# Kernel optimization log

Hardware: AMD Instinct MI355X
Metric: run time of the kernel (lower is better)

Reference implementation:

```python
import jax, jax.numpy as jnp
import numpy as np

GAMMA = 0.96875
SCALE_BASE = 512.0


def _fixed_pos_embedding(scale):
    # scale: (L, d) where d = head_dim // 2
    L, d = scale.shape
    inv_freq = 1.0 / (10000.0 ** (jnp.arange(d, dtype=jnp.float32) / d))
    sinusoid = jnp.arange(L, dtype=jnp.float32)[:, None] * inv_freq  # (L, d)
    return jnp.sin(sinusoid), jnp.cos(sinusoid)


def _rotate_every_two(x):
    # (..., D) -> (..., D) with pairs (x0, x1) -> (-x1, x0)
    x1 = x[..., ::2]
    x2 = x[..., 1::2]
    return jnp.stack((-x2, x1), axis=-1).reshape(x.shape)


def _dup_interleave(m):
    # (L, d) -> (L, 2d), each column duplicated (matches rotary pairing)
    return jnp.repeat(m, 2, axis=-1)


def xpos(x, offset=0, downscale=False):
    # x: (B, S, D). Standard torchscale-style XPos rotary embedding.
    S, D = x.shape[-2], x.shape[-1]
    scale_vec = (jnp.arange(0, D, 2, dtype=jnp.float32) + 0.4 * D) / (1.4 * D)  # (D/2,)
    min_pos = -(S + offset) // 2
    max_pos = S + offset + min_pos
    power = jnp.arange(min_pos, max_pos, dtype=jnp.float32) / SCALE_BASE  # (S+offset,)
    scale = scale_vec ** power[:, None]  # (S+offset, D/2)
    sin, cos = _fixed_pos_embedding(scale)
    if scale.shape[0] > S:  # keep the last S positions
        scale, sin, cos = scale[-S:], sin[-S:], cos[-S:]
    if downscale:
        scale = 1.0 / scale
    sin = _dup_interleave(sin * scale)  # (S, D)
    cos = _dup_interleave(cos * scale)  # (S, D)
    return x * cos + _rotate_every_two(x) * sin


def _decay_mask(S, dtype):
    # D[n, m] = gamma^(n-m) if n >= m else 0  (lower triangular)
    m = jnp.arange(S)
    diff = m[:, None] - m  # (S, S)
    causal = diff >= 0
    exp = jnp.where(causal, diff, 0).astype(dtype)
    return jnp.where(causal, jnp.asarray(GAMMA, dtype) ** exp, jnp.zeros((), dtype))


def setup_inputs() -> dict:
    key = jax.random.key(0)
    kx, kq, kk, kv = jax.random.split(key, 4)
    B, S, H, Dh = 4, 4096, 2048, 256
    return {
        "x": jax.random.normal(kx, (B, S, H), dtype=jnp.float32),
        "w_q": jax.random.normal(kq, (H, Dh), dtype=jnp.float32),
        "w_k": jax.random.normal(kk, (H, Dh), dtype=jnp.float32),
        "w_v": jax.random.normal(kv, (H, Dh), dtype=jnp.float32),
    }


def reference(x, w_q, w_k, w_v):
    # x: (B, S, H) -> out: (B, S, Dh)
    B, S, _ = x.shape
    decay = _decay_mask(S, x.dtype)[None]  # (1, S, S)
    q = xpos(x @ w_q)                       # (B, S, Dh)
    k = xpos(x @ w_k, downscale=True)       # (B, S, Dh)
    v = x @ w_v                             # (B, S, Dh)
    ret = jnp.einsum("bsd,btd->bst", q, k) * decay  # (B, S, S)
    return jnp.einsum("bst,btd->bsd", ret, v)       # (B, S, Dh)
```

## Files before the change

### kernel.cpp

```cpp
#include <hip/hip_runtime.h>
#include <cstddef>
#include <cstdint>

#define Bn 4
#define Sn 4096
#define Hn 2048
#define Dn 256

typedef float f32x16 __attribute__((ext_vector_type(16)));
typedef short bf16x8 __attribute__((ext_vector_type(8)));

#define AS3 __attribute__((address_space(3)))
#define AS1 __attribute__((address_space(1)))

#define L2G -0.045803689613125f
#define GC 2.9526131e-4f

__device__ __forceinline__ unsigned short f2bf(float f) {
  union { float f; unsigned int u; } a; a.f = f;
  unsigned int r = a.u + 0x7fffu + ((a.u >> 16) & 1u);
  return (unsigned short)(r >> 16);
}
__device__ __forceinline__ float bf2f(unsigned int b) {
  union { unsigned int u; float f; } a; a.u = b << 16;
  return a.f;
}

__global__ __launch_bounds__(256) void prep_kernel(const float* __restrict__ x,
                                                   const float* __restrict__ wq,
                                                   const float* __restrict__ wk,
                                                   const float* __restrict__ wv,
                                                   unsigned short* __restrict__ xb,
                                                   unsigned short* __restrict__ wt,
                                                   float* __restrict__ rt) {
  __shared__ __align__(16) unsigned short T[64][72];
  const int bx = blockIdx.x;
  const int tid = threadIdx.x;
  if (bx < 2048) {
    const int g = bx * 256 + tid;
    const int s = g >> 7;
    const int jp = g & 127;
    const float invf = exp2f((float)jp * (-13.287712379549449f / 128.0f));
    float sn, cs;
    sincosf((float)s * invf, &sn, &cs);
    const float l2sv = log2f((2.0f * jp + 102.4f) * (1.0f / 358.4f));
    const float pw = ((float)s - 2048.0f) * (1.0f / 512.0f);
    const float tl = (float)(s & 255) * L2G;
    const float ex = pw * l2sv + tl;
    const float eq = exp2f(ex), ek = exp2f(-ex);
    float2* q = (float2*)rt;
    float2* k = (float2*)(rt + 4096 * 256);
    q[(size_t)s * 128 + jp] = make_float2(cs * eq, sn * eq);
    k[(size_t)s * 128 + jp] = make_float2(cs * ek, sn * ek);
  } else if (bx < 10240) {
    const size_t g = (size_t)(bx - 2048) * 256 + tid;
    const float* src = x + g * 16;
    unsigned short* dst = xb + g * 16;
    uint4 o0, o1;
    float4 v0 = ((const float4*)src)[0];
    float4 v1 = ((const float4*)src)[1];
    float4 v2 = ((const float4*)src)[2];
    float4 v3 = ((const float4*)src)[3];
    o0.x = f2bf(v0.x) | ((unsigned int)f2bf(v0.y) << 16);
    o0.y = f2bf(v0.z) | ((unsigned int)f2bf(v0.w) << 16);
    o0.z = f2bf(v1.x) | ((unsigned int)f2bf(v1.y) << 16);
    o0.w = f2bf(v1.z) | ((unsigned int)f2bf(v1.w) << 16);
    o1.x = f2bf(v2.x) | ((unsigned int)f2bf(v2.y) << 16);
    o1.y = f2bf(v2.z) | ((unsigned int)f2bf(v2.w) << 16);
    o1.z = f2bf(v3.x) | ((unsigned int)f2bf(v3.y) << 16);
    o1.w = f2bf(v3.z) | ((unsigned int)f2bf(v3.w) << 16);
    ((uint4*)dst)[0] = o0;
    ((uint4*)dst)[1] = o1;
  } else {
    const int bw = bx - 10240;
    const int k0 = (bw & 31) * 64;
    const int n0 = (bw >> 5) * 64;
    const float* w = (n0 < 256) ? wq : (n0 < 512 ? wk : wv);
    const int nc0 = n0 & 255;
#pragma unroll
    for (int it = 0; it < 2; ++it) {
      int flat = it * 256 + tid;
      int r = flat >> 3, c8 = flat & 7;
      const float* src = w + (size_t)(k0 + r) * 256 + nc0 + c8 * 8;
      float4 v0 = *(const float4*)src;
      float4 v1 = *(const float4*)(src + 4);
      T[c8 * 8 + 0][r] = f2bf(v0.x); T[c8 * 8 + 1][r] = f2bf(v0.y);
      T[c8 * 8 + 2][r] = f2bf(v0.z); T[c8 * 8 + 3][r] = f2bf(v0.w);
      T[c8 * 8 + 4][r] = f2bf(v1.x); T[c8 * 8 + 5][r] = f2bf(v1.y);
      T[c8 * 8 + 6][r] = f2bf(v1.z); T[c8 * 8 + 7][r] = f2bf(v1.w);
    }
    __syncthreads();
#pragma unroll
    for (int it = 0; it < 2; ++it) {
      int flat = it * 256 + tid;
      int nr = flat >> 3, kc8 = flat & 7;
      int n = n0 + nr;
      int kc_sw = kc8 ^ (n & 7);
      uint4 val = *(const uint4*)&T[nr][kc8 * 8];
      *(uint4*)((char*)wt + (size_t)n * 4096 + (size_t)k0 * 2 + kc_sw * 16) = val;
    }
  }
}

__global__ __launch_bounds__(512, 2) void proj4_kernel(const unsigned short* __restrict__ xb,
                                                       const unsigned short* __restrict__ wt,
                                                       const float* __restrict__ rt,
                                                       unsigned short* __restrict__ qkv,
                                                       unsigned short* __restrict__ kt,
                                                       unsigned short* __restrict__ vt) {
  __shared__ __align__(16) char smem[49152];
  unsigned short* As = (unsigned short*)smem;
  unsigned short* Bs = (unsigned short*)(smem + 16384);
  const int tid = threadIdx.x;
  const int lane = tid & 63;
  const int wid = tid >> 6;
  const int wr = wid >> 2, wc = wid & 3;
  const int m0 = blockIdx.x * 128;
  const int kind = blockIdx.y;
  const int l31 = lane & 31, lh = lane >> 5;

  f32x16 acc[2][2];
#pragma unroll
  for (int i = 0; i < 2; ++i)
#pragma unroll
    for (int j = 0; j < 2; ++j) acc[i][j] = 0.0f;

  for (int k0 = 0; k0 < Hn; k0 += 64) {
    AS3 char* ldsa = (AS3 char*)As;
    AS3 char* ldsb = (AS3 char*)Bs;
#pragma unroll
    for (int i = 0; i < 2; ++i) {
      int ou = i * 8192 + wid * 1024;
      int o = ou + lane * 16;
      int row = o >> 7, colB = o & 127;
      const char* srcA = (const char*)xb + (size_t)(m0 + row) * 4096 + k0 * 2 + (colB ^ ((row & 7) << 4));
      __builtin_amdgcn_global_load_lds((const AS1 unsigned int*)srcA,
                                       (AS3 unsigned int*)(ldsa + ou), 16, 0, 0);
    }
#pragma unroll
    for (int i = 0; i < 4; ++i) {
      int ou = i * 8192 + wid * 1024;
      int o = ou + lane * 16;
      int row = o >> 7, colB = o & 127;
      const char* srcB = (const char*)wt + (size_t)(kind * 256 + row) * 4096 + k0 * 2 + colB;
      __builtin_amdgcn_global_load_lds((const AS1 unsigned int*)srcB,
                                       (AS3 unsigned int*)(ldsb + ou), 16, 0, 0);
    }
    __syncthreads();
#pragma unroll
    for (int kc = 0; kc < 4; ++kc) {
      const int kb = kc * 32 + lh * 16;
      bf16x8 a[2], b[2];
#pragma unroll
      for (int i = 0; i < 2; ++i) {
        int mr = wr * 64 + i * 32 + l31;
        a[i] = *(const bf16x8*)((const char*)As + mr * 128 + (kb ^ ((mr & 7) << 4)));
        int nr = wc * 64 + i * 32 + l31;
        b[i] = *(const bf16x8*)((const char*)Bs + nr * 128 + (kb ^ ((nr & 7) << 4)));
      }
#pragma unroll
      for (int i = 0; i < 2; ++i)
#pragma unroll
        for (int j = 0; j < 2; ++j)
          acc[i][j] = __builtin_amdgcn_mfma_f32_32x32x16_bf16(a[i], b[j], acc[i][j], 0, 0, 0);
    }
    __syncthreads();
  }

  const int bidx = m0 >> 12;
  const int t0b = m0 & 4095;

  if (kind < 2) {
    const float* rtb = rt + (size_t)kind * (4096 * 256);
    int jp[2];
#pragma unroll
    for (int j = 0; j < 2; ++j) jp[j] = (wc * 64 + j * 32 + l31) >> 1;
    const int odd = l31 & 1;
#pragma unroll
    for (int i = 0; i < 2; ++i)
#pragma unroll
      for (int reg = 0; reg < 16; ++reg) {
        const int mm = m0 + wr * 64 + i * 32 + (reg & 3) + 8 * (reg >> 2) + 4 * lh;
        const int s = mm & (Sn - 1);
#pragma unroll
        for (int j = 0; j < 2; ++j) {
          const float2 cf = *(const float2*)(rtb + (size_t)s * 256 + jp[j] * 2);
          float v = acc[i][j][reg];
          float p = __shfl_xor(v, 1, 64);
          acc[i][j][reg] = odd ? (v * cf.x + p * cf.y) : (v * cf.x - p * cf.y);
        }
      }
  }

  if (kind == 0) {
#pragma unroll
    for (int i = 0; i < 2; ++i)
#pragma unroll
      for (int j = 0; j < 2; ++j)
#pragma unroll
        for (int reg = 0; reg < 16; ++reg) {
          int m = m0 + wr * 64 + i * 32 + (reg & 3) + 8 * (reg >> 2) + 4 * lh;
          int n = wc * 64 + j * 32 + l31;
          qkv[(size_t)m * 768 + n] = f2bf(acc[i][j][reg]);
        }
  } else {
    if (kind == 1) {
#pragma unroll
      for (int i = 0; i < 2; ++i)
#pragma unroll
        for (int j = 0; j < 2; ++j)
#pragma unroll
          for (int reg = 0; reg < 16; ++reg) {
            int m = m0 + wr * 64 + i * 32 + (reg & 3) + 8 * (reg >> 2) + 4 * lh;
            int d = wc * 64 + j * 32 + l31;
            qkv[(size_t)m * 768 + 256 + (d ^ ((m & 7) << 3))] = f2bf(acc[i][j][reg]);
          }
    }
    unsigned short* dst = (kind == 1) ? kt : vt;
#pragma unroll
    for (int h = 0; h < 2; ++h) {
      __syncthreads();
      if ((wc >> 1) == h) {
#pragma unroll
        for (int i = 0; i < 2; ++i)
#pragma unroll
          for (int j = 0; j < 2; ++j) {
            const int dl = (wc & 1) * 64 + j * 32 + l31;
#pragma unroll
            for (int k8 = 0; k8 < 8; ++k8) {
              const int r0 = 2 * k8;
              const int t = wr * 64 + i * 32 + (r0 & 3) + 8 * (r0 >> 2) + 4 * lh;
              unsigned int pk;
              asm("v_cvt_pk_bf16_f32 %0, %1, %2" : "=v"(pk)
                  : "v"(acc[i][j][r0]), "v"(acc[i][j][r0 + 1]));
              *(unsigned int*)(smem + dl * 256 + ((2 * t) ^ ((dl & 7) << 4))) = pk;
            }
          }
      }
      __syncthreads();
#pragma unroll
      for (int p = 0; p < 4; ++p) {
        const int fl = p * 512 + tid;
        const int dl = fl >> 4, t8 = fl & 15;
        uint4 val = *(const uint4*)(smem + dl * 256 + ((t8 * 16) ^ ((dl & 7) << 4)));
        *(uint4*)(dst + (size_t)(bidx * 256 + h * 128 + dl) * 4096 + t0b + t8 * 8) = val;
      }
    }
  }
}

__global__ __launch_bounds__(256) void wt_build(const float* __restrict__ wq,
                                                const float* __restrict__ wk,
                                                const float* __restrict__ wv,
                                                unsigned short* __restrict__ wt) {
  __shared__ __align__(16) unsigned short T[64][72];
  const int tid = threadIdx.x;
  const int k0 = blockIdx.x * 64;
  const int n0 = blockIdx.y * 64;
  const float* w = (n0 < 256) ? wq : (n0 < 512 ? wk : wv);
  const int nc0 = n0 & 255;
#pragma unroll
  for (int it = 0; it < 2; ++it) {
    int flat = it * 256 + tid;
    int r = flat >> 3, c8 = flat & 7;
    const float* src = w + (size_t)(k0 + r) * 256 + nc0 + c8 * 8;
    float4 v0 = *(const float4*)src;
    float4 v1 = *(const float4*)(src + 4);
    T[c8 * 8 + 0][r] = f2bf(v0.x); T[c8 * 8 + 1][r] = f2bf(v0.y);
    T[c8 * 8 + 2][r] = f2bf(v0.z); T[c8 * 8 + 3][r] = f2bf(v0.w);
    T[c8 * 8 + 4][r] = f2bf(v1.x); T[c8 * 8 + 5][r] = f2bf(v1.y);
    T[c8 * 8 + 6][r] = f2bf(v1.z); T[c8 * 8 + 7][r] = f2bf(v1.w);
  }
  __syncthreads();
#pragma unroll
  for (int it = 0; it < 2; ++it) {
    int flat = it * 256 + tid;
    int nr = flat >> 3, kc8 = flat & 7;
    int n = n0 + nr;
    int kc_sw = kc8 ^ (n & 7);
    uint4 val = *(const uint4*)&T[nr][kc8 * 8];
    *(uint4*)((char*)wt + (size_t)n * 4096 + (size_t)k0 * 2 + kc_sw * 16) = val;
  }
}

__global__ __launch_bounds__(256, 2) void proj_kernel(const float* __restrict__ x,
                                                      const unsigned short* __restrict__ wt,
                                                      unsigned short* __restrict__ qkv) {
  __shared__ __align__(16) unsigned short As[128 * 64];
  __shared__ __align__(16) unsigned short Bs[128 * 64];
  const int tid = threadIdx.x;
  const int lane = tid & 63;
  const int wid = tid >> 6;
  const int wr = wid >> 1, wc = wid & 1;
  const int m0 = blockIdx.x * 128;
  const int n0 = blockIdx.y * 128;
  const int l31 = lane & 31, lh = lane >> 5;

  f32x16 acc[2][2];
#pragma unroll
  for (int i = 0; i < 2; ++i)
#pragma unroll
    for (int j = 0; j < 2; ++j) acc[i][j] = 0.0f;

  for (int k0 = 0; k0 < Hn; k0 += 64) {
    {
      AS3 char* ldsb = (AS3 char*)Bs;
#pragma unroll
      for (int i = 0; i < 4; ++i) {
        int ou = i * 4096 + wid * 1024;
        int o = ou + lane * 16;
        int row = o >> 7, col = o & 127;
        const char* src = (const char*)wt + (size_t)(n0 + row) * 4096 + k0 * 2 + col;
        __builtin_amdgcn_global_load_lds((const AS1 unsigned int*)src,
                                         (AS3 unsigned int*)(ldsb + ou), 16, 0, 0);
      }
    }
#pragma unroll
    for (int i = 0; i < 4; ++i) {
      int o = i * 256 + tid;
      int row = o >> 3, c8 = o & 7;
      const float* src = x + (size_t)(m0 + row) * 2048 + k0 + c8 * 8;
      float4 v0 = *(const float4*)src;
      float4 v1 = *(const float4*)(src + 4);
      uint4 val;
      val.x = f2bf(v0.x) | ((unsigned int)f2bf(v0.y) << 16);
      val.y = f2bf(v0.z) | ((unsigned int)f2bf(v0.w) << 16);
      val.z = f2bf(v1.x) | ((unsigned int)f2bf(v1.y) << 16);
      val.w = f2bf(v1.z) | ((unsigned int)f2bf(v1.w) << 16);
      *(uint4*)((char*)As + row * 128 + ((c8 * 16) ^ ((row & 7) << 4))) = val;
    }
    __syncthreads();
#pragma unroll
    for (int kc = 0; kc < 4; ++kc) {
      const int kb = kc * 32 + lh * 16;
      bf16x8 a[2], b[2];
#pragma unroll
      for (int i = 0; i < 2; ++i) {
        int mr = wr * 64 + i * 32 + l31;
        a[i] = *(const bf16x8*)((const char*)As + mr * 128 + (kb ^ ((mr & 7) << 4)));
        int nr = wc * 64 + i * 32 + l31;
        b[i] = *(const bf16x8*)((const char*)Bs + nr * 128 + (kb ^ ((nr & 7) << 4)));
      }
#pragma unroll
      for (int i = 0; i < 2; ++i)
#pragma unroll
        for (int j = 0; j < 2; ++j)
          acc[i][j] = __builtin_amdgcn_mfma_f32_32x32x16_bf16(a[i], b[j], acc[i][j], 0, 0, 0);
    }
    __syncthreads();
  }
  const bool khalf = (n0 >= 256 && n0 < 512);
#pragma unroll
  for (int i = 0; i < 2; ++i)
#pragma unroll
    for (int j = 0; j < 2; ++j)
#pragma unroll
      for (int reg = 0; reg < 16; ++reg) {
        int m = m0 + wr * 64 + i * 32 + (reg & 3) + 8 * (reg >> 2) + 4 * lh;
        int n = n0 + wc * 64 + j * 32 + l31;
        if (khalf) n = 256 + ((n - 256) ^ ((m & 7) << 3));
        qkv[(size_t)m * 768 + n] = f2bf(acc[i][j][reg]);
      }
}

__global__ __launch_bounds__(256) void xpos_kernel(unsigned short* __restrict__ qkv) {
  const int g = blockIdx.x * 256 + threadIdx.x;
  const int m = g >> 5;
  const int c = g & 31;
  const float s = (float)(m & (Sn - 1));
  unsigned short* qrow = qkv + (size_t)m * 768;
  const int csw = c ^ (m & 7);
  uint4 qv = *(uint4*)(qrow + c * 8);
  uint4 kv = *(uint4*)(qrow + 256 + csw * 8);
  unsigned int* qu = (unsigned int*)&qv;
  unsigned int* ku = (unsigned int*)&kv;
  const float pw = (s - 2048.0f) * (1.0f / 512.0f);
  const float gp = exp2f((float)(m & 255) * L2G);
#pragma unroll
  for (int p = 0; p < 4; ++p) {
    const int jp = c * 4 + p;
    const float invf = exp2f((float)jp * (-13.287712379549449f / 128.0f));
    float sn, cs;
    sincosf(s * invf, &sn, &cs);
    const float sv = (2.0f * jp + 102.4f) * (1.0f / 358.4f);
    const float scq = exp2f(pw * log2f(sv)) * gp;
    const float sci = 1.0f / scq;
    float q0 = bf2f(qu[p] & 0xffffu), q1 = bf2f(qu[p] >> 16);
    float k0 = bf2f(ku[p] & 0xffffu), k1 = bf2f(ku[p] >> 16);
    float q0r = (q0 * cs - q1 * sn) * scq;
    float q1r = (q1 * cs + q0 * sn) * scq;
    float k0r = (k0 * cs - k1 * sn) * sci;
    float k1r = (k1 * cs + k0 * sn) * sci;
    qu[p] = f2bf(q0r) | ((unsigned int)f2bf(q1r) << 16);
    ku[p] = f2bf(k0r) | ((unsigned int)f2bf(k1r) << 16);
  }
  *(uint4*)(qrow + c * 8) = qv;
  *(uint4*)(qrow + 256 + csw * 8) = kv;
}

__global__ __launch_bounds__(256) void kvt_build(const unsigned short* __restrict__ qkv,
                                                 unsigned short* __restrict__ kt,
                                                 unsigned short* __restrict__ vt) {
  __shared__ __align__(16) unsigned short Tk[64][72];
  __shared__ __align__(16) unsigned short Tv[64][72];
  const int tid = threadIdx.x;
  const int t0 = blockIdx.x * 64;
  const int d0 = blockIdx.y * 64;
  const int b = blockIdx.z;
  const size_t rowb = ((size_t)b * Sn + t0) * 1536;
#pragma unroll
  for (int it = 0; it < 2; ++it) {
    int flat = it * 256 + tid;
    int r = flat >> 3, c8 = flat & 7;
    int kc = (d0 >> 3) + c8;
    int kcs = kc ^ (r & 7);
    uint4 kvv = *(const uint4*)((const char*)qkv + rowb + (size_t)r * 1536 + 512 + kcs * 16);
    uint4 vvv = *(const uint4*)((const char*)qkv + rowb + (size_t)r * 1536 + 1024 + (size_t)(d0 + c8 * 8) * 2);
    const unsigned short* ke = (const unsigned short*)&kvv;
    const unsigned short* ve = (const unsigned short*)&vvv;
#pragma unroll
    for (int e = 0; e < 8; ++e) { Tk[c8 * 8 + e][r] = ke[e]; Tv[c8 * 8 + e][r] = ve[e]; }
  }
  __syncthreads();
#pragma unroll
  for (int it = 0; it < 2; ++it) {
    int flat = it * 256 + tid;
    int dr = flat >> 3, tc8 = flat & 7;
    *(uint4*)(kt + (size_t)(b * 256 + d0 + dr) * 4096 + t0 + tc8 * 8) = *(const uint4*)&Tk[dr][tc8 * 8];
    *(uint4*)(vt + (size_t)(b * 256 + d0 + dr) * 4096 + t0 + tc8 * 8) = *(const uint4*)&Tv[dr][tc8 * 8];
  }
}

__global__ __launch_bounds__(256) void mbuild_kernel(const unsigned short* __restrict__ kt,
                                                     const unsigned short* __restrict__ vt,
                                                     unsigned short* __restrict__ mt) {
  const int tid = threadIdx.x;
  const int lane = tid & 63;
  const int wid = tid >> 6;
  const int l31 = lane & 31, lh = lane >> 5;
  const int jc = blockIdx.x;
  const int quad = blockIdx.y;
  const int b = blockIdx.z;
  const int d2w = ((quad >> 1) * 2 + (wid >> 1)) * 64;
  const int d1w = ((quad & 1) * 2 + (wid & 1)) * 64;
  const size_t tb = (size_t)jc * 256;

  f32x16 acc[2][2];
#pragma unroll
  for (int i = 0; i < 2; ++i)
#pragma unroll
    for (int j = 0; j < 2; ++j) acc[i][j] = 0.0f;

#pragma unroll 2
  for (int dc = 0; dc < 16; ++dc) {
    const int ko = dc * 32 + lh * 16;
    bf16x8 a[2], bb[2];
#pragma unroll
    for (int i = 0; i < 2; ++i) {
      a[i]  = *(const bf16x8*)((const char*)vt + ((size_t)(b * 256 + d2w + i * 32 + l31) * 4096 + tb) * 2 + ko);
      bb[i] = *(const bf16x8*)((const char*)kt + ((size_t)(b * 256 + d1w + i * 32 + l31) * 4096 + tb) * 2 + ko);
    }
#pragma unroll
    for (int i = 0; i < 2; ++i)
#pragma unroll
      for (int j = 0; j < 2; ++j)
        acc[i][j] = __builtin_amdgcn_mfma_f32_32x32x16_bf16(a[i], bb[j], acc[i][j], 0, 0, 0);
  }
  unsigned short* dst = mt + ((size_t)(b * 16 + jc) << 16);
#pragma unroll
  for (int i = 0; i < 2; ++i)
#pragma unroll
    for (int j = 0; j < 2; ++j)
#pragma unroll
      for (int reg = 0; reg < 16; ++reg) {
        int row = d2w + i * 32 + (reg & 3) + 8 * (reg >> 2) + 4 * lh;
        int col = d1w + j * 32 + l31;
        dst[row * 256 + col] = f2bf(acc[i][j][reg]);
      }
}

__global__ __launch_bounds__(256) void scan_kernel(unsigned short* __restrict__ mt) {
  const int e0 = (blockIdx.x * 256 + threadIdx.x) * 4;
  const int b = blockIdx.y;
  unsigned short* base = mt + ((size_t)b << 20);
  float s0 = 0.f, s1 = 0.f, s2 = 0.f, s3 = 0.f;
  for (int j = 1; j < 16; ++j) {
    unsigned short* p = base + ((size_t)(j - 1) << 16) + e0;
    uint2 mv = *(const uint2*)p;
    s0 = GC * (s0 + bf2f(mv.x & 0xffffu));
    s1 = GC * (s1 + bf2f(mv.x >> 16));
    s2 = GC * (s2 + bf2f(mv.y & 0xffffu));
    s3 = GC * (s3 + bf2f(mv.y >> 16));
    uint2 w;
    w.x = f2bf(s0) | ((unsigned int)f2bf(s1) << 16);
    w.y = f2bf(s2) | ((unsigned int)f2bf(s3) << 16);
    *(uint2*)p = w;
  }
}

__global__ __launch_bounds__(256, 2) void retc_kernel(const unsigned short* __restrict__ qkv,
                                                      const unsigned short* __restrict__ vt,
                                                      const unsigned short* __restrict__ mt,
                                                      float* __restrict__ out) {
  __shared__ float cmb[2][32][128];
  const int tid = threadIdx.x;
  const int lane = tid & 63;
  const int tw = tid >> 6;
  const int l31 = lane & 31, lh = lane >> 5;
  const int st = blockIdx.x;
  const int dh = blockIdx.y;
  const int b = blockIdx.z;
  const int j = st >> 3;
  const int base = st & ~7;
  const int s0 = st * 32;
  const int d0 = dh * 128;

  bf16x8 qf[16];
  {
    const char* qrow = (const char*)qkv + ((size_t)b * Sn + s0 + l31) * 1536;
#pragma unroll
    for (int dc = 0; dc < 16; ++dc)
      qf[dc] = *(const bf16x8*)(qrow + dc * 32 + lh * 16);
  }

  f32x16 acc[4];
#pragma unroll
  for (int i = 0; i < 4; ++i) acc[i] = 0.0f;

  if (j > 0) {
    const char* Sj = (const char*)mt + ((size_t)(b * 16 + j - 1) << 17);
#pragma unroll
    for (int dcl = 0; dcl < 4; ++dcl) {
      const int dc = tw * 4 + dcl;
#pragma unroll
      for (int g = 0; g < 4; ++g) {
        const int d2 = d0 + g * 32 + l31;
        bf16x8 sbf = *(const bf16x8*)(Sj + (size_t)d2 * 512 + dc * 32 + lh * 16);
        acc[g] = __builtin_amdgcn_mfma_f32_32x32x16_bf16(qf[dc], sbf, acc[g], 0, 0, 0);
      }
    }
  }

  const int sg = s0 + l31;
  const int ksw = (l31 & 7) << 4;
  for (int tt = base; tt <= st; ++tt) {
    if (((tt - base) & 3) != tw) continue;
    const bool msk = (tt == st);
    const int t0 = tt * 32;

    f32x16 sacc = 0.0f;
    const char* krow = (const char*)qkv + ((size_t)b * Sn + t0 + l31) * 1536 + 512;
    __builtin_amdgcn_s_setprio(1);
#pragma unroll
    for (int dc = 0; dc < 16; ++dc) {
      bf16x8 kf = *(const bf16x8*)(krow + ((dc * 32 + lh * 16) ^ ksw));
      sacc = __builtin_amdgcn_mfma_f32_32x32x16_bf16(kf, qf[dc], sacc, 0, 0, 0);
    }
    __builtin_amdgcn_s_setprio(0);

    unsigned int P[8];
#pragma unroll
    for (int k = 0; k < 8; ++k) {
      const int r0 = 2 * k;
      float f0 = sacc[r0], f1 = sacc[r0 + 1];
      if (msk) {
        const int tg0 = t0 + (r0 & 3) + 8 * (r0 >> 2) + 4 * lh;
        f0 = (sg - tg0 >= 0) ? f0 : 0.0f;
        f1 = (sg - tg0 - 1 >= 0) ? f1 : 0.0f;
      }
      unsigned int pk;
      asm("v_cvt_pk_bf16_f32 %0, %1, %2" : "=v"(pk) : "v"(f0), "v"(f1));
      P[k] = pk;
    }
    asm volatile("v_permlane32_swap_b32 %0, %1" : "+v"(P[0]), "+v"(P[2]));
    asm volatile("v_permlane32_swap_b32 %0, %1" : "+v"(P[1]), "+v"(P[3]));
    asm volatile("v_permlane32_swap_b32 %0, %1" : "+v"(P[4]), "+v"(P[6]));
    asm volatile("v_permlane32_swap_b32 %0, %1" : "+v"(P[5]), "+v"(P[7]));

    __builtin_amdgcn_s_setprio(1);
#pragma unroll
    for (int kc = 0; kc < 2; ++kc) {
      uint4 pw;
      pw.x = P[kc * 4 + 0]; pw.y = P[kc * 4 + 1];
      pw.z = P[kc * 4 + 2]; pw.w = P[kc * 4 + 3];
      bf16x8 pf = *(const bf16x8*)&pw;
#pragma unroll
      for (int g = 0; g < 4; ++g) {
        const int d = d0 + g * 32 + l31;
        bf16x8 vf = *(const bf16x8*)((const char*)vt +
            ((size_t)(b * 256 + d) * 4096 + t0) * 2 + kc * 32 + lh * 16);
        acc[g] = __builtin_amdgcn_mfma_f32_32x32x16_bf16(pf, vf, acc[g], 0, 0, 0);
      }
    }
    __builtin_amdgcn_s_setprio(0);
  }

  if (tw >= 2) {
#pragma unroll
    for (int g = 0; g < 4; ++g)
#pragma unroll
      for (int reg = 0; reg < 16; ++reg) {
        int sl = (reg & 3) + 8 * (reg >> 2) + 4 * lh;
        cmb[tw - 2][sl][g * 32 + l31] = acc[g][reg];
      }
  }
  __syncthreads();
  if (tw < 2) {
#pragma unroll
    for (int g = 0; g < 4; ++g)
#pragma unroll
      for (int reg = 0; reg < 16; ++reg) {
        int sl = (reg & 3) + 8 * (reg >> 2) + 4 * lh;
        acc[g][reg] += cmb[tw][sl][g * 32 + l31];
      }
  }
  __syncthreads();
  if (tw == 1) {
#pragma unroll
    for (int g = 0; g < 4; ++g)
#pragma unroll
      for (int reg = 0; reg < 16; ++reg) {
        int sl = (reg & 3) + 8 * (reg >> 2) + 4 * lh;
        cmb[0][sl][g * 32 + l31] = acc[g][reg];
      }
  }
  __syncthreads();
  if (tw == 0) {
#pragma unroll
    for (int g = 0; g < 4; ++g)
#pragma unroll
      for (int reg = 0; reg < 16; ++reg) {
        int sl = (reg & 3) + 8 * (reg >> 2) + 4 * lh;
        int c = g * 32 + l31;
        out[((size_t)(b * Sn + s0 + sl)) * 256 + d0 + c] = acc[g][reg] + cmb[0][sl][c];
      }
  }
}

extern "C" void kernel_launch(void* const* d_in, const int* in_sizes, int n_in,
                              void* d_out, int out_size, void* d_ws, size_t ws_size,
                              hipStream_t stream) {
  (void)in_sizes; (void)n_in; (void)out_size;
  const float* x  = (const float*)d_in[0];
  const float* wq = (const float*)d_in[1];
  const float* wk = (const float*)d_in[2];
  const float* wv = (const float*)d_in[3];
  float* out = (float*)d_out;
  char* ws = (char*)d_ws;

  unsigned short* qkv = (unsigned short*)(ws);
  unsigned short* vt  = (unsigned short*)(ws + 25165824);
  unsigned short* kt  = (unsigned short*)(ws + 33554432);
  unsigned short* mt  = (unsigned short*)(ws + 41943040);

  const size_t NEED_BIG = 128974848;
  if (ws_size >= NEED_BIG) {
    unsigned short* xb = (unsigned short*)(ws + 50331648);
    unsigned short* wt = (unsigned short*)(ws + 117440512);
    float*          rtab = (float*)(ws + 120586240);
    prep_kernel<<<10624, 256, 0, stream>>>(x, wq, wk, wv, xb, wt, rtab);
    proj4_kernel<<<dim3(128, 3), 512, 0, stream>>>(xb, wt, rtab, qkv, kt, vt);
  } else {
    unsigned short* wt = (unsigned short*)(ws + 41943040);
    wt_build<<<dim3(32, 12), 256, 0, stream>>>(wq, wk, wv, wt);
    proj_kernel<<<dim3(128, 6), 256, 0, stream>>>(x, wt, qkv);
    xpos_kernel<<<2048, 256, 0, stream>>>(qkv);
    kvt_build<<<dim3(64, 4, 4), 256, 0, stream>>>(qkv, kt, vt);
  }
  mbuild_kernel<<<dim3(16, 4, 4), 256, 0, stream>>>(kt, vt, mt);
  scan_kernel<<<dim3(64, 4), 256, 0, stream>>>(mt);
  retc_kernel<<<dim3(128, 2, 4), 256, 0, stream>>>(qkv, vt, mt, out);
}
```

Before: 176.3 us.

## Triple-buffer LDS in projection GEMM with async global-to-LDS prefetch

Turns the projection kernel's single-buffered K loop into a three-stage pipeline. Tiles for steps t+1 and t+2 load asynchronously through global_load_lds into separate LDS buffers while MFMAs run on step t, gated by explicit vmcnt waits and raw barriers. It also raises wave priority around the MFMA block. LDS use grows to 144KB per block, which likely drops occupancy from two blocks per CU to one, and the hand-counted vmcnt values must match the number of loads issued per stage.

```diff
diff --git a/kernel.cpp b/kernel.cpp
--- a/kernel.cpp
+++ b/kernel.cpp
@@ -102,15 +102,13 @@
   }
 }
 
-__global__ __launch_bounds__(512, 2) void proj4_kernel(const unsigned short* __restrict__ xb,
+__global__ __launch_bounds__(512, 2) void proj5_kernel(const unsigned short* __restrict__ xb,
                                                        const unsigned short* __restrict__ wt,
                                                        const float* __restrict__ rt,
                                                        unsigned short* __restrict__ qkv,
                                                        unsigned short* __restrict__ kt,
                                                        unsigned short* __restrict__ vt) {
-  __shared__ __align__(16) char smem[49152];
-  unsigned short* As = (unsigned short*)smem;
-  unsigned short* Bs = (unsigned short*)(smem + 16384);
+  __shared__ __align__(16) char smem[147456];
   const int tid = threadIdx.x;
   const int lane = tid & 63;
   const int wid = tid >> 6;
@@ -119,15 +117,10 @@
   const int kind = blockIdx.y;
   const int l31 = lane & 31, lh = lane >> 5;
 
-  f32x16 acc[2][2];
-#pragma unroll
-  for (int i = 0; i < 2; ++i)
-#pragma unroll
-    for (int j = 0; j < 2; ++j) acc[i][j] = 0.0f;
-
-  for (int k0 = 0; k0 < Hn; k0 += 64) {
-    AS3 char* ldsa = (AS3 char*)As;
-    AS3 char* ldsb = (AS3 char*)Bs;
+  auto STAGE = [&](int buf, int kt) {
+    AS3 char* ldsa = (AS3 char*)(smem + buf * 49152);
+    AS3 char* ldsb = ldsa + 16384;
+    const int k0 = kt * 64;
 #pragma unroll
     for (int i = 0; i < 2; ++i) {
       int ou = i * 8192 + wid * 1024;
@@ -146,7 +139,28 @@
       __builtin_amdgcn_global_load_lds((const AS1 unsigned int*)srcB,
                                        (AS3 unsigned int*)(ldsb + ou), 16, 0, 0);
     }
-    __syncthreads();
+  };
+
+  f32x16 acc[2][2];
+#pragma unroll
+  for (int i = 0; i < 2; ++i)
+#pragma unroll
+    for (int j = 0; j < 2; ++j) acc[i][j] = 0.0f;
+
+  STAGE(0, 0);
+  STAGE(1, 1);
+  STAGE(2, 2);
+
+  int buf = 0;
+  for (int t = 0; t < 32; ++t) {
+    if (t < 30)       asm volatile("s_waitcnt vmcnt(12)" ::: "memory");
+    else if (t == 30) asm volatile("s_waitcnt vmcnt(6)" ::: "memory");
+    else              asm volatile("s_waitcnt vmcnt(0)" ::: "memory");
+    __builtin_amdgcn_s_barrier();
+
+    const char* Asb = smem + buf * 49152;
+    const char* Bsb = Asb + 16384;
+    __builtin_amdgcn_s_setprio(1);
 #pragma unroll
     for (int kc = 0; kc < 4; ++kc) {
       const int kb = kc * 32 + lh * 16;
@@ -154,9 +168,9 @@
 #pragma unroll
       for (int i = 0; i < 2; ++i) {
         int mr = wr * 64 + i * 32 + l31;
-        a[i] = *(const bf16x8*)((const char*)As + mr * 128 + (kb ^ ((mr & 7) << 4)));
+        a[i] = *(const bf16x8*)(Asb + mr * 128 + (kb ^ ((mr & 7) << 4)));
         int nr = wc * 64 + i * 32 + l31;
-        b[i] = *(const bf16x8*)((const char*)Bs + nr * 128 + (kb ^ ((nr & 7) << 4)));
+        b[i] = *(const bf16x8*)(Bsb + nr * 128 + (kb ^ ((nr & 7) << 4)));
       }
 #pragma unroll
       for (int i = 0; i < 2; ++i)
@@ -164,7 +178,11 @@
         for (int j = 0; j < 2; ++j)
           acc[i][j] = __builtin_amdgcn_mfma_f32_32x32x16_bf16(a[i], b[j], acc[i][j], 0, 0, 0);
     }
-    __syncthreads();
+    __builtin_amdgcn_s_setprio(0);
+
+    __builtin_amdgcn_s_barrier();
+    if (t + 3 < 32) STAGE(buf, t + 3);
+    buf = (buf == 2) ? 0 : buf + 1;
   }
 
   const int bidx = m0 >> 12;
@@ -659,7 +677,7 @@
     unsigned short* wt = (unsigned short*)(ws + 117440512);
     float*          rtab = (float*)(ws + 120586240);
     prep_kernel<<<10624, 256, 0, stream>>>(x, wq, wk, wv, xb, wt, rtab);
-    proj4_kernel<<<dim3(128, 3), 512, 0, stream>>>(xb, wt, rtab, qkv, kt, vt);
+    proj5_kernel<<<dim3(128, 3), 512, 0, stream>>>(xb, wt, rtab, qkv, kt, vt);
   } else {
     unsigned short* wt = (unsigned short*)(ws + 41943040);
     wt_build<<<dim3(32, 12), 256, 0, stream>>>(wq, wk, wv, wt);
```

After: 188.6 us. 7.0% more time.

## Fuse x fp32-to-bf16 conversion into projection GEMM A-tile load

Applied to the files above, without the earlier changes.

Removes the separate pass that converted x to bf16 in the prep kernel. The projection kernel now loads fp32 x directly into registers, converts with packed bf16 instructions, and writes swizzled tiles to LDS. This avoids writing and re-reading a 64MB bf16 copy of x. The cost is that x is read in fp32 by each of the 3 kind blocks (3x 128MB) instead of bf16, and the A path loses its async global_load_lds, so loads now stall the waves synchronously.

```diff
diff --git a/kernel.cpp b/kernel.cpp
--- a/kernel.cpp
+++ b/kernel.cpp
@@ -26,11 +26,9 @@
   return a.f;
 }
 
-__global__ __launch_bounds__(256) void prep_kernel(const float* __restrict__ x,
-                                                   const float* __restrict__ wq,
+__global__ __launch_bounds__(256) void prep_kernel(const float* __restrict__ wq,
                                                    const float* __restrict__ wk,
                                                    const float* __restrict__ wv,
-                                                   unsigned short* __restrict__ xb,
                                                    unsigned short* __restrict__ wt,
                                                    float* __restrict__ rt) {
   __shared__ __align__(16) unsigned short T[64][72];
@@ -52,27 +50,8 @@
     float2* k = (float2*)(rt + 4096 * 256);
     q[(size_t)s * 128 + jp] = make_float2(cs * eq, sn * eq);
     k[(size_t)s * 128 + jp] = make_float2(cs * ek, sn * ek);
-  } else if (bx < 10240) {
-    const size_t g = (size_t)(bx - 2048) * 256 + tid;
-    const float* src = x + g * 16;
-    unsigned short* dst = xb + g * 16;
-    uint4 o0, o1;
-    float4 v0 = ((const float4*)src)[0];
-    float4 v1 = ((const float4*)src)[1];
-    float4 v2 = ((const float4*)src)[2];
-    float4 v3 = ((const float4*)src)[3];
-    o0.x = f2bf(v0.x) | ((unsigned int)f2bf(v0.y) << 16);
-    o0.y = f2bf(v0.z) | ((unsigned int)f2bf(v0.w) << 16);
-    o0.z = f2bf(v1.x) | ((unsigned int)f2bf(v1.y) << 16);
-    o0.w = f2bf(v1.z) | ((unsigned int)f2bf(v1.w) << 16);
-    o1.x = f2bf(v2.x) | ((unsigned int)f2bf(v2.y) << 16);
-    o1.y = f2bf(v2.z) | ((unsigned int)f2bf(v2.w) << 16);
-    o1.z = f2bf(v3.x) | ((unsigned int)f2bf(v3.y) << 16);
-    o1.w = f2bf(v3.z) | ((unsigned int)f2bf(v3.w) << 16);
-    ((uint4*)dst)[0] = o0;
-    ((uint4*)dst)[1] = o1;
   } else {
-    const int bw = bx - 10240;
+    const int bw = bx - 2048;
     const int k0 = (bw & 31) * 64;
     const int n0 = (bw >> 5) * 64;
     const float* w = (n0 < 256) ? wq : (n0 < 512 ? wk : wv);
@@ -102,7 +81,7 @@
   }
 }
 
-__global__ __launch_bounds__(512, 2) void proj4_kernel(const unsigned short* __restrict__ xb,
+__global__ __launch_bounds__(512, 2) void proj6_kernel(const float* __restrict__ x,
                                                        const unsigned short* __restrict__ wt,
                                                        const float* __restrict__ rt,
                                                        unsigned short* __restrict__ qkv,
@@ -110,7 +89,6 @@
                                                        unsigned short* __restrict__ vt) {
   __shared__ __align__(16) char smem[49152];
   unsigned short* As = (unsigned short*)smem;
-  unsigned short* Bs = (unsigned short*)(smem + 16384);
   const int tid = threadIdx.x;
   const int lane = tid & 63;
   const int wid = tid >> 6;
@@ -119,6 +97,10 @@
   const int kind = blockIdx.y;
   const int l31 = lane & 31, lh = lane >> 5;
 
+  const int arow = tid >> 2;
+  const int acg = (tid & 3) << 4;
+  const int asw = (arow & 7) << 4;
+
   f32x16 acc[2][2];
 #pragma unroll
   for (int i = 0; i < 2; ++i)
@@ -126,25 +108,35 @@
     for (int j = 0; j < 2; ++j) acc[i][j] = 0.0f;
 
   for (int k0 = 0; k0 < Hn; k0 += 64) {
-    AS3 char* ldsa = (AS3 char*)As;
-    AS3 char* ldsb = (AS3 char*)Bs;
-#pragma unroll
-    for (int i = 0; i < 2; ++i) {
-      int ou = i * 8192 + wid * 1024;
-      int o = ou + lane * 16;
-      int row = o >> 7, colB = o & 127;
-      const char* srcA = (const char*)xb + (size_t)(m0 + row) * 4096 + k0 * 2 + (colB ^ ((row & 7) << 4));
-      __builtin_amdgcn_global_load_lds((const AS1 unsigned int*)srcA,
-                                       (AS3 unsigned int*)(ldsa + ou), 16, 0, 0);
-    }
-#pragma unroll
-    for (int i = 0; i < 4; ++i) {
-      int ou = i * 8192 + wid * 1024;
-      int o = ou + lane * 16;
-      int row = o >> 7, colB = o & 127;
-      const char* srcB = (const char*)wt + (size_t)(kind * 256 + row) * 4096 + k0 * 2 + colB;
-      __builtin_amdgcn_global_load_lds((const AS1 unsigned int*)srcB,
-                                       (AS3 unsigned int*)(ldsb + ou), 16, 0, 0);
+    const float* srcA = x + (size_t)(m0 + arow) * 2048 + k0 + acg;
+    float4 f0 = ((const float4*)srcA)[0];
+    float4 f1 = ((const float4*)srcA)[1];
+    float4 f2 = ((const float4*)srcA)[2];
+    float4 f3 = ((const float4*)srcA)[3];
+    {
+      AS3 char* ldsb = (AS3 char*)(smem + 16384);
+#pragma unroll
+      for (int i = 0; i < 4; ++i) {
+        int ou = i * 8192 + wid * 1024;
+        int o = ou + lane * 16;
+        int row = o >> 7, colB = o & 127;
+        const char* srcB = (const char*)wt + (size_t)(kind * 256 + row) * 4096 + k0 * 2 + colB;
+        __builtin_amdgcn_global_load_lds((const AS1 unsigned int*)srcB,
+                                         (AS3 unsigned int*)(ldsb + ou), 16, 0, 0);
+      }
+    }
+    {
+      uint4 u0, u1;
+      asm("v_cvt_pk_bf16_f32 %0, %1, %2" : "=v"(u0.x) : "v"(f0.x), "v"(f0.y));
+      asm("v_cvt_pk_bf16_f32 %0, %1, %2" : "=v"(u0.y) : "v"(f0.z), "v"(f0.w));
+      asm("v_cvt_pk_bf16_f32 %0, %1, %2" : "=v"(u0.z) : "v"(f1.x), "v"(f1.y));
+      asm("v_cvt_pk_bf16_f32 %0, %1, %2" : "=v"(u0.w) : "v"(f1.z), "v"(f1.w));
+      asm("v_cvt_pk_bf16_f32 %0, %1, %2" : "=v"(u1.x) : "v"(f2.x), "v"(f2.y));
+      asm("v_cvt_pk_bf16_f32 %0, %1, %2" : "=v"(u1.y) : "v"(f2.z), "v"(f2.w));
+      asm("v_cvt_pk_bf16_f32 %0, %1, %2" : "=v"(u1.z) : "v"(f3.x), "v"(f3.y));
+      asm("v_cvt_pk_bf16_f32 %0, %1, %2" : "=v"(u1.w) : "v"(f3.z), "v"(f3.w));
+      *(uint4*)((char*)As + arow * 128 + ((acg * 2) ^ asw)) = u0;
+      *(uint4*)((char*)As + arow * 128 + ((acg * 2 + 16) ^ asw)) = u1;
     }
     __syncthreads();
 #pragma unroll
@@ -156,7 +148,7 @@
         int mr = wr * 64 + i * 32 + l31;
         a[i] = *(const bf16x8*)((const char*)As + mr * 128 + (kb ^ ((mr & 7) << 4)));
         int nr = wc * 64 + i * 32 + l31;
-        b[i] = *(const bf16x8*)((const char*)Bs + nr * 128 + (kb ^ ((nr & 7) << 4)));
+        b[i] = *(const bf16x8*)(smem + 16384 + nr * 128 + (kb ^ ((nr & 7) << 4)));
       }
 #pragma unroll
       for (int i = 0; i < 2; ++i)
@@ -655,11 +647,10 @@
 
   const size_t NEED_BIG = 128974848;
   if (ws_size >= NEED_BIG) {
-    unsigned short* xb = (unsigned short*)(ws + 50331648);
     unsigned short* wt = (unsigned short*)(ws + 117440512);
     float*          rtab = (float*)(ws + 120586240);
-    prep_kernel<<<10624, 256, 0, stream>>>(x, wq, wk, wv, xb, wt, rtab);
-    proj4_kernel<<<dim3(128, 3), 512, 0, stream>>>(xb, wt, rtab, qkv, kt, vt);
+    prep_kernel<<<2432, 256, 0, stream>>>(wq, wk, wv, wt, rtab);
+    proj6_kernel<<<dim3(128, 3), 512, 0, stream>>>(x, wt, rtab, qkv, kt, vt);
   } else {
     unsigned short* wt = (unsigned short*)(ws + 41943040);
     wt_build<<<dim3(32, 12), 256, 0, stream>>>(wq, wk, wv, wt);
```

After: 162.2 us, median of 4. -8.0%, faster.
